# Kernel tuning notes

Measured on AMD Instinct MI355X. Metric: run time of the kernel, lower is better.

The kernel has to match this reference:

```python
import jax, jax.numpy as jnp
import numpy as np

N_VARS = 32        # n_variables
TEMPERATURE = 1.0  # softmax temperature (default)


def setup_inputs() -> dict:
    key = jax.random.key(0)
    k1, k2 = jax.random.split(key)
    B, C, T = 16, 3072, 2048  # C = n_var * (hidden_dim + n_var) = 32*(64+32)
    x = jax.random.normal(k1, (B, C, T), dtype=jnp.float32)
    x_instant = jax.random.normal(k2, (B, C, T), dtype=jnp.float32)
    return {"x": x, "x_instant": x_instant}


def _split_context_attention(v, n):
    B, _, T = v.shape
    v = v.reshape(B, n, -1, T)          # (B, n, hidden+n, T)
    attn = v[:, :, :n, :]               # (B, n, n, T) attention logits
    ctx = v[:, :, n:, :]                # (B, n, hidden, T)
    return ctx, attn


def reference(x, x_instant):
    n = N_VARS
    B, _, T = x.shape
    ctx, attn = _split_context_attention(x, n)
    ctx_i, attn_i = _split_context_attention(x_instant, n)
    ctx = jnp.concatenate([ctx, ctx_i], axis=-3)     # (B, 2n, hidden, T)
    attn = jnp.concatenate([attn, attn_i], axis=-2)  # (B, n, 2n, T)
    attn = jax.nn.softmax(attn / TEMPERATURE, axis=-2)
    # aggregate contexts with attention weights
    out = jnp.einsum('bijt,bjdt->bidt', attn, ctx)   # (B, n, hidden, T)
    out = out.reshape(B, -1, T)                      # (B, n*hidden, T)
    # ConvertInstant: zero the instantaneous self-edge (j = n + i), then sum chunks
    a1 = attn[:, :, :n, :]
    a2 = attn[:, :, n:, :]
    diag = jnp.eye(n, dtype=bool)[None, :, :, None]  # (1, n, n, 1)
    a2 = jnp.where(diag, jnp.zeros((), dtype=attn.dtype), a2)
    attentions = a1 + a2                             # (B, n, n, T)
    return out, attentions
```

## Files before the change

kernel.cpp:

```cpp
#include <hip/hip_runtime.h>
#include <stdint.h>


typedef unsigned int uint_t;
typedef float  f32x4   __attribute__((ext_vector_type(4)));
typedef short  short8v __attribute__((ext_vector_type(8)));

#define SYNCX() asm volatile("s_waitcnt lgkmcnt(0)\n\ts_barrier" ::: "memory")

constexpr int Bq = 16, Cq = 3072, Tq = 2048;
constexpr int TT = 32, TILES = 64, NBLK = Bq * TILES;
constexpr size_t ATT_OFF = (size_t)Bq * 2048 * Tq;
constexpr int TBS = 4224;
constexpr int LDS_BYTES = 135168;

__global__ __launch_bounds__(1024, 1) void attn_v14(const float* __restrict__ x,
                                                    const float* __restrict__ xi,
                                                    float* __restrict__ out)
{
    __shared__ __align__(16) unsigned char smem[LDS_BYTES];
    uint_t*    LW = (uint_t*)smem;
    uint64_t*  LQ = (uint64_t*)smem;
    float*     LF = (float*)smem;

    const int tid  = (int)threadIdx.x;
    const int b    = (int)blockIdx.x >> 6;
    const int tile = (int)blockIdx.x & (TILES - 1);
    const int t0   = tile * TT;
    const int tl   = tid & 31;
    const int slot = tid >> 5;

    const float* xb  = x  + (size_t)b * Cq * Tq + t0 + tl;
    const float* xib = xi + (size_t)b * Cq * Tq + t0 + tl;

    uint_t pk[32];
    float  cre[32];

    auto issue = [&](int c) {
        const int dh = c >> 1, jh = c & 1;
        const float* src = (jh == 0) ? x : xi;
        const float* sp  = src + (size_t)b * Cq * Tq
                         + (size_t)(32 + dh * 32 + slot) * Tq + t0 + tl;
#pragma unroll
        for (int kk = 0; kk < 32; ++kk) cre[kk] = sp[(size_t)kk * 96 * Tq];
    };

    {
        const int i = slot;
        float p[64];
#pragma unroll
        for (int j = 0; j < 32; ++j) p[j]      = xb [(size_t)(i * 96 + j) * Tq];
#pragma unroll
        for (int j = 0; j < 32; ++j) p[j + 32] = xib[(size_t)(i * 96 + j) * Tq];

        issue(0);

        float m = p[0];
#pragma unroll
        for (int j = 1; j < 64; ++j) m = fmaxf(m, p[j]);
        float s = 0.f;
#pragma unroll
        for (int j = 0; j < 64; ++j) { p[j] = __expf(p[j] - m); s += p[j]; }
        const float inv = 1.f / s;
#pragma unroll
        for (int j = 0; j < 64; ++j) p[j] *= inv;

        float* ao = out + ATT_OFF + ((size_t)(b * 32 + i) * 32) * Tq + t0 + tl;
#pragma unroll
        for (int j = 0; j < 32; ++j) {
            float v = p[j] + ((j == i) ? 0.f : p[j + 32]);
            __builtin_nontemporal_store(v, &ao[(size_t)j * Tq]);
        }
#pragma unroll
        for (int k = 0; k < 32; ++k) {
            uint_t b0 = __float_as_uint(p[2 * k]);
            uint_t b1 = __float_as_uint(p[2 * k + 1]);
            uint_t lo = (b0 + 0x7fffu + ((b0 >> 16) & 1u)) >> 16;
            uint_t hi = (b1 + 0x7fffu + ((b1 >> 16) & 1u)) >> 16;
            pk[k] = lo | (hi << 16);
        }
    }

    const int fw  = ((slot >> 2) & 3) ^ (slot & 3);
    const int TBw = tl * TBS + (tl & 7) * 16;

    const int l   = tid & 63;
    const int wv  = tid >> 6;
    const int frd = ((l >> 2) & 3) ^ (l & 3);
    const int kbr = (((l >> 4) ^ frd) & 3) * 16;
    const int rA  = (l & 15) * 64;

    auto stageP = [&](int jh) {
#pragma unroll
        for (int m = 0; m < 16; m += 2) {
            const int kbx  = (m >> 2) ^ fw;
            const int byte = TBw + slot * 64 + kbx * 16 + ((2 * m) & 7) * 2;
            uint64_t w = (uint64_t)pk[jh * 16 + m] |
                         ((uint64_t)pk[jh * 16 + m + 1] << 32);
            LQ[byte >> 3] = w;
        }
    };
    auto stageC = [&]() {
#pragma unroll
        for (int kk = 0; kk < 32; kk += 2) {
            uint_t b0 = __float_as_uint(cre[kk]);
            uint_t b1 = __float_as_uint(cre[kk + 1]);
            uint_t h0 = (b0 + 0x7fffu + ((b0 >> 16) & 1u)) >> 16;
            uint_t h1 = (b1 + 0x7fffu + ((b1 >> 16) & 1u)) >> 16;
            const int kbx  = (kk >> 3) ^ fw;
            const int byte = TBw + 2048 + slot * 64 + kbx * 16 + (kk & 7) * 2;
            LW[byte >> 2] = h0 | (h1 << 16);
        }
    };

    f32x4 acc[2][2][2];
    auto accClr = [&]() {
#pragma unroll
        for (int q = 0; q < 2; ++q)
#pragma unroll
            for (int s = 0; s < 2; ++s)
#pragma unroll
                for (int dt = 0; dt < 2; ++dt) acc[q][s][dt] = (f32x4)(0.f);
    };
    auto mfmaChunk = [&]() {
#pragma unroll
        for (int q = 0; q < 2; ++q) {
            const int tloc = 2 * wv + q;
            const int base = tloc * TBS + (tloc & 7) * 16;
            const short8v A0 = *(const short8v*)(smem + base        + rA + kbr);
            const short8v A1 = *(const short8v*)(smem + base + 1024 + rA + kbr);
            const short8v B0 = *(const short8v*)(smem + base + 2048 + rA + kbr);
            const short8v B1 = *(const short8v*)(smem + base + 3072 + rA + kbr);
            acc[q][0][0] = __builtin_amdgcn_mfma_f32_16x16x32_bf16(A0, B0, acc[q][0][0], 0, 0, 0);
            acc[q][0][1] = __builtin_amdgcn_mfma_f32_16x16x32_bf16(A0, B1, acc[q][0][1], 0, 0, 0);
            acc[q][1][0] = __builtin_amdgcn_mfma_f32_16x16x32_bf16(A1, B0, acc[q][1][0], 0, 0, 0);
            acc[q][1][1] = __builtin_amdgcn_mfma_f32_16x16x32_bf16(A1, B1, acc[q][1][1], 0, 0, 0);
        }
    };
    auto dump = [&](int dh) {
#pragma unroll
        for (int q = 0; q < 2; ++q)
#pragma unroll
            for (int s = 0; s < 2; ++s)
#pragma unroll
                for (int dt = 0; dt < 2; ++dt)
#pragma unroll
                    for (int ri = 0; ri < 4; ++ri) {
                        const int ii = s * 16 + (l >> 4) * 4 + ri;
                        const int dl = dt * 16 + (l & 15);
                        LF[(ii * 32 + dl) * 33 + 2 * wv + q] = acc[q][s][dt][ri];
                    }
        SYNCX();
        float* ob = out + (size_t)b * 2048 * Tq + t0 + tl;
#pragma unroll 8
        for (int kk = 0; kk < 32; ++kk) {
            const int ch = kk * 64 + dh * 32 + slot;
            __builtin_nontemporal_store(LF[(kk * 32 + slot) * 33 + tl],
                                        &ob[(size_t)ch * Tq]);
        }
        SYNCX();
    };

    accClr();
    stageP(0); stageC();
    SYNCX();
    issue(1);
    mfmaChunk();
    SYNCX();
    stageP(1); stageC();
    SYNCX();
    issue(2);
    mfmaChunk();
    SYNCX();
    dump(0);
    accClr();
    stageP(0); stageC();
    SYNCX();
    issue(3);
    mfmaChunk();
    SYNCX();
    stageP(1); stageC();
    SYNCX();
    mfmaChunk();
    SYNCX();
    dump(1);
}

extern "C" void kernel_launch(void* const* d_in, const int* in_sizes, int n_in,
                              void* d_out, int out_size, void* d_ws, size_t ws_size,
                              hipStream_t stream) {
    const float* x  = (const float*)d_in[0];
    const float* xi = (const float*)d_in[1];
    float* out = (float*)d_out;
    attn_v14<<<dim3(NBLK), dim3(1024), 0, stream>>>(x, xi, out);
}
```

Baseline: 258.9 us.

## Double-buffer LDS staging by time-half to overlap staging with MFMA

Splits the 32 time columns into two halves of 16 and stages each half into a separate LDS buffer, so one half can be written while MFMAs read the other half. Each wave now handles one time column per half instead of two consecutive ones, and the accumulator index maps to the time half. The aim is to hide LDS staging latency and the barrier stalls between staging and compute. In exchange there are more barriers and the staging work per step is split across half the threads, which leaves the other threads idle during those stores.

Measured after the change: 275.9 us. 1.07x slower.

```diff
diff --git a/kernel.cpp b/kernel.cpp
--- a/kernel.cpp
+++ b/kernel.cpp
@@ -12,9 +12,10 @@
 constexpr int TT = 32, TILES = 64, NBLK = Bq * TILES;
 constexpr size_t ATT_OFF = (size_t)Bq * 2048 * Tq;
 constexpr int TBS = 4224;
-constexpr int LDS_BYTES = 135168;
-
-__global__ __launch_bounds__(1024, 1) void attn_v14(const float* __restrict__ x,
+constexpr int BB  = 16 * TBS;
+constexpr int LDS_BYTES = 2 * BB;
+
+__global__ __launch_bounds__(1024, 1) void attn_v16(const float* __restrict__ x,
                                                     const float* __restrict__ xi,
                                                     float* __restrict__ out)
 {
@@ -36,8 +37,8 @@
     uint_t pk[32];
     float  cre[32];
 
-    auto issue = [&](int c) {
-        const int dh = c >> 1, jh = c & 1;
+    auto issueQ = [&](int q) {
+        const int dh = q >> 1, jh = q & 1;
         const float* src = (jh == 0) ? x : xi;
         const float* sp  = src + (size_t)b * Cq * Tq
                          + (size_t)(32 + dh * 32 + slot) * Tq + t0 + tl;
@@ -53,7 +54,7 @@
 #pragma unroll
         for (int j = 0; j < 32; ++j) p[j + 32] = xib[(size_t)(i * 96 + j) * Tq];
 
-        issue(0);
+        issueQ(0);
 
         float m = p[0];
 #pragma unroll
@@ -82,25 +83,30 @@
     }
 
     const int fw  = ((slot >> 2) & 3) ^ (slot & 3);
-    const int TBw = tl * TBS + (tl & 7) * 16;
+    const int tau = tl & 15;
+    const int thh = tl >> 4;
+    const int TBw = tau * TBS + (tau & 7) * 16;
 
     const int l   = tid & 63;
     const int wv  = tid >> 6;
     const int frd = ((l >> 2) & 3) ^ (l & 3);
     const int kbr = (((l >> 4) ^ frd) & 3) * 16;
     const int rA  = (l & 15) * 64;
-
-    auto stageP = [&](int jh) {
+    const int mb  = wv * TBS + (wv & 7) * 16;
+
+    auto stageP = [&](int jh, int th, int buf) {
+        if (thh != th) return;
 #pragma unroll
         for (int m = 0; m < 16; m += 2) {
             const int kbx  = (m >> 2) ^ fw;
-            const int byte = TBw + slot * 64 + kbx * 16 + ((2 * m) & 7) * 2;
+            const int byte = buf * BB + TBw + slot * 64 + kbx * 16 + ((2 * m) & 7) * 2;
             uint64_t w = (uint64_t)pk[jh * 16 + m] |
                          ((uint64_t)pk[jh * 16 + m + 1] << 32);
             LQ[byte >> 3] = w;
         }
     };
-    auto stageC = [&]() {
+    auto stageC = [&](int th, int buf) {
+        if (thh != th) return;
 #pragma unroll
         for (int kk = 0; kk < 32; kk += 2) {
             uint_t b0 = __float_as_uint(cre[kk]);
@@ -108,7 +114,7 @@
             uint_t h0 = (b0 + 0x7fffu + ((b0 >> 16) & 1u)) >> 16;
             uint_t h1 = (b1 + 0x7fffu + ((b1 >> 16) & 1u)) >> 16;
             const int kbx  = (kk >> 3) ^ fw;
-            const int byte = TBw + 2048 + slot * 64 + kbx * 16 + (kk & 7) * 2;
+            const int byte = buf * BB + TBw + 2048 + slot * 64 + kbx * 16 + (kk & 7) * 2;
             LW[byte >> 2] = h0 | (h1 << 16);
         }
     };
@@ -122,24 +128,20 @@
 #pragma unroll
                 for (int dt = 0; dt < 2; ++dt) acc[q][s][dt] = (f32x4)(0.f);
     };
-    auto mfmaChunk = [&]() {
-#pragma unroll
-        for (int q = 0; q < 2; ++q) {
-            const int tloc = 2 * wv + q;
-            const int base = tloc * TBS + (tloc & 7) * 16;
-            const short8v A0 = *(const short8v*)(smem + base        + rA + kbr);
-            const short8v A1 = *(const short8v*)(smem + base + 1024 + rA + kbr);
-            const short8v B0 = *(const short8v*)(smem + base + 2048 + rA + kbr);
-            const short8v B1 = *(const short8v*)(smem + base + 3072 + rA + kbr);
-            acc[q][0][0] = __builtin_amdgcn_mfma_f32_16x16x32_bf16(A0, B0, acc[q][0][0], 0, 0, 0);
-            acc[q][0][1] = __builtin_amdgcn_mfma_f32_16x16x32_bf16(A0, B1, acc[q][0][1], 0, 0, 0);
-            acc[q][1][0] = __builtin_amdgcn_mfma_f32_16x16x32_bf16(A1, B0, acc[q][1][0], 0, 0, 0);
-            acc[q][1][1] = __builtin_amdgcn_mfma_f32_16x16x32_bf16(A1, B1, acc[q][1][1], 0, 0, 0);
-        }
-    };
-    auto dump = [&](int dh) {
-#pragma unroll
-        for (int q = 0; q < 2; ++q)
+    auto mfmaC = [&](int th, int buf) {
+        const int base = buf * BB + mb;
+        const short8v A0 = *(const short8v*)(smem + base        + rA + kbr);
+        const short8v A1 = *(const short8v*)(smem + base + 1024 + rA + kbr);
+        const short8v B0 = *(const short8v*)(smem + base + 2048 + rA + kbr);
+        const short8v B1 = *(const short8v*)(smem + base + 3072 + rA + kbr);
+        acc[th][0][0] = __builtin_amdgcn_mfma_f32_16x16x32_bf16(A0, B0, acc[th][0][0], 0, 0, 0);
+        acc[th][0][1] = __builtin_amdgcn_mfma_f32_16x16x32_bf16(A0, B1, acc[th][0][1], 0, 0, 0);
+        acc[th][1][0] = __builtin_amdgcn_mfma_f32_16x16x32_bf16(A1, B0, acc[th][1][0], 0, 0, 0);
+        acc[th][1][1] = __builtin_amdgcn_mfma_f32_16x16x32_bf16(A1, B1, acc[th][1][1], 0, 0, 0);
+    };
+    auto dumpW = [&]() {
+#pragma unroll
+        for (int th = 0; th < 2; ++th)
 #pragma unroll
             for (int s = 0; s < 2; ++s)
 #pragma unroll
@@ -148,9 +150,10 @@
                     for (int ri = 0; ri < 4; ++ri) {
                         const int ii = s * 16 + (l >> 4) * 4 + ri;
                         const int dl = dt * 16 + (l & 15);
-                        LF[(ii * 32 + dl) * 33 + 2 * wv + q] = acc[q][s][dt][ri];
+                        LF[(ii * 32 + dl) * 33 + th * 16 + wv] = acc[th][s][dt][ri];
                     }
-        SYNCX();
+    };
+    auto dumpS = [&](int dh) {
         float* ob = out + (size_t)b * 2048 * Tq + t0 + tl;
 #pragma unroll 8
         for (int kk = 0; kk < 32; ++kk) {
@@ -158,32 +161,41 @@
             __builtin_nontemporal_store(LF[(kk * 32 + slot) * 33 + tl],
                                         &ob[(size_t)ch * Tq]);
         }
-        SYNCX();
     };
 
     accClr();
-    stageP(0); stageC();
-    SYNCX();
-    issue(1);
-    mfmaChunk();
-    SYNCX();
-    stageP(1); stageC();
-    SYNCX();
-    issue(2);
-    mfmaChunk();
-    SYNCX();
-    dump(0);
+    stageP(0, 0, 0); stageC(0, 0);
+    SYNCX();
+    stageP(0, 1, 1); stageC(1, 1);
+    issueQ(1);
+    mfmaC(0, 0);
+    SYNCX();
+    stageP(1, 0, 0); stageC(0, 0);
+    mfmaC(1, 1);
+    SYNCX();
+    stageP(1, 1, 1); stageC(1, 1);
+    issueQ(2);
+    mfmaC(0, 0);
+    SYNCX();
+    mfmaC(1, 1);
+    SYNCX();
+    dumpW(); SYNCX(); dumpS(0); SYNCX();
     accClr();
-    stageP(0); stageC();
-    SYNCX();
-    issue(3);
-    mfmaChunk();
-    SYNCX();
-    stageP(1); stageC();
-    SYNCX();
-    mfmaChunk();
-    SYNCX();
-    dump(1);
+    stageP(0, 0, 0); stageC(0, 0);
+    SYNCX();
+    stageP(0, 1, 1); stageC(1, 1);
+    issueQ(3);
+    mfmaC(0, 0);
+    SYNCX();
+    stageP(1, 0, 0); stageC(0, 0);
+    mfmaC(1, 1);
+    SYNCX();
+    stageP(1, 1, 1); stageC(1, 1);
+    mfmaC(0, 0);
+    SYNCX();
+    mfmaC(1, 1);
+    SYNCX();
+    dumpW(); SYNCX(); dumpS(1);
 }
 
 extern "C" void kernel_launch(void* const* d_in, const int* in_sizes, int n_in,
@@ -192,5 +204,5 @@
     const float* x  = (const float*)d_in[0];
     const float* xi = (const float*)d_in[1];
     float* out = (float*)d_out;
-    attn_v14<<<dim3(NBLK), dim3(1024), 0, stream>>>(x, xi, out);
+    attn_v16<<<dim3(NBLK), dim3(1024), 0, stream>>>(x, xi, out);
 }
```

## Make kernel persistent with 512 threads processing four tiles and prefetching logits

Applied to the files above, without the earlier changes.

Shrinks the grid to 256 blocks of 512 threads. Each block loops over four (batch, time-tile) units, and each thread handles two attention rows and two context channels per stage. The next tile's logits are prefetched during the last MFMA stage to overlap global loads with compute, and fewer blocks cut launch and tail costs. In exchange, register pressure per thread roughly doubles, there are fewer waves per CU to hide latency, and the first stageC loads cre from x for both halves before issueQ reloads it.

After: 400.1 us. +54.5%, slower.

```diff
diff --git a/kernel.cpp b/kernel.cpp
--- a/kernel.cpp
+++ b/kernel.cpp
@@ -9,14 +9,15 @@
 #define SYNCX() asm volatile("s_waitcnt lgkmcnt(0)\n\ts_barrier" ::: "memory")
 
 constexpr int Bq = 16, Cq = 3072, Tq = 2048;
-constexpr int TT = 32, TILES = 64, NBLK = Bq * TILES;
+constexpr int TT = 32, TILES = 64;
+constexpr int NBLK = 256;
 constexpr size_t ATT_OFF = (size_t)Bq * 2048 * Tq;
 constexpr int TBS = 4224;
 constexpr int LDS_BYTES = 135168;
 
-__global__ __launch_bounds__(1024, 1) void attn_v14(const float* __restrict__ x,
-                                                    const float* __restrict__ xi,
-                                                    float* __restrict__ out)
+__global__ __launch_bounds__(512, 1) void attn_v17(const float* __restrict__ x,
+                                                   const float* __restrict__ xi,
+                                                   float* __restrict__ out)
 {
     __shared__ __align__(16) unsigned char smem[LDS_BYTES];
     uint_t*    LW = (uint_t*)smem;
@@ -24,62 +25,9 @@
     float*     LF = (float*)smem;
 
     const int tid  = (int)threadIdx.x;
-    const int b    = (int)blockIdx.x >> 6;
-    const int tile = (int)blockIdx.x & (TILES - 1);
-    const int t0   = tile * TT;
     const int tl   = tid & 31;
     const int slot = tid >> 5;
-
-    const float* xb  = x  + (size_t)b * Cq * Tq + t0 + tl;
-    const float* xib = xi + (size_t)b * Cq * Tq + t0 + tl;
-
-    uint_t pk[32];
-    float  cre[32];
-
-    auto issue = [&](int c) {
-        const int dh = c >> 1, jh = c & 1;
-        const float* src = (jh == 0) ? x : xi;
-        const float* sp  = src + (size_t)b * Cq * Tq
-                         + (size_t)(32 + dh * 32 + slot) * Tq + t0 + tl;
-#pragma unroll
-        for (int kk = 0; kk < 32; ++kk) cre[kk] = sp[(size_t)kk * 96 * Tq];
-    };
-
-    {
-        const int i = slot;
-        float p[64];
-#pragma unroll
-        for (int j = 0; j < 32; ++j) p[j]      = xb [(size_t)(i * 96 + j) * Tq];
-#pragma unroll
-        for (int j = 0; j < 32; ++j) p[j + 32] = xib[(size_t)(i * 96 + j) * Tq];
-
-        issue(0);
-
-        float m = p[0];
-#pragma unroll
-        for (int j = 1; j < 64; ++j) m = fmaxf(m, p[j]);
-        float s = 0.f;
-#pragma unroll
-        for (int j = 0; j < 64; ++j) { p[j] = __expf(p[j] - m); s += p[j]; }
-        const float inv = 1.f / s;
-#pragma unroll
-        for (int j = 0; j < 64; ++j) p[j] *= inv;
-
-        float* ao = out + ATT_OFF + ((size_t)(b * 32 + i) * 32) * Tq + t0 + tl;
-#pragma unroll
-        for (int j = 0; j < 32; ++j) {
-            float v = p[j] + ((j == i) ? 0.f : p[j + 32]);
-            __builtin_nontemporal_store(v, &ao[(size_t)j * Tq]);
-        }
-#pragma unroll
-        for (int k = 0; k < 32; ++k) {
-            uint_t b0 = __float_as_uint(p[2 * k]);
-            uint_t b1 = __float_as_uint(p[2 * k + 1]);
-            uint_t lo = (b0 + 0x7fffu + ((b0 >> 16) & 1u)) >> 16;
-            uint_t hi = (b1 + 0x7fffu + ((b1 >> 16) & 1u)) >> 16;
-            pk[k] = lo | (hi << 16);
-        }
-    }
+    const int blk  = (int)blockIdx.x;
 
     const int fw  = ((slot >> 2) & 3) ^ (slot & 3);
     const int TBw = tl * TBS + (tl & 7) * 16;
@@ -90,100 +38,222 @@
     const int kbr = (((l >> 4) ^ frd) & 3) * 16;
     const int rA  = (l & 15) * 64;
 
-    auto stageP = [&](int jh) {
-#pragma unroll
-        for (int m = 0; m < 16; m += 2) {
-            const int kbx  = (m >> 2) ^ fw;
-            const int byte = TBw + slot * 64 + kbx * 16 + ((2 * m) & 7) * 2;
-            uint64_t w = (uint64_t)pk[jh * 16 + m] |
-                         ((uint64_t)pk[jh * 16 + m + 1] << 32);
-            LQ[byte >> 3] = w;
-        }
-    };
-    auto stageC = [&]() {
-#pragma unroll
-        for (int kk = 0; kk < 32; kk += 2) {
-            uint_t b0 = __float_as_uint(cre[kk]);
-            uint_t b1 = __float_as_uint(cre[kk + 1]);
-            uint_t h0 = (b0 + 0x7fffu + ((b0 >> 16) & 1u)) >> 16;
-            uint_t h1 = (b1 + 0x7fffu + ((b1 >> 16) & 1u)) >> 16;
-            const int kbx  = (kk >> 3) ^ fw;
-            const int byte = TBw + 2048 + slot * 64 + kbx * 16 + (kk & 7) * 2;
-            LW[byte >> 2] = h0 | (h1 << 16);
-        }
-    };
-
-    f32x4 acc[2][2][2];
-    auto accClr = [&]() {
-#pragma unroll
-        for (int q = 0; q < 2; ++q)
-#pragma unroll
-            for (int s = 0; s < 2; ++s)
-#pragma unroll
-                for (int dt = 0; dt < 2; ++dt) acc[q][s][dt] = (f32x4)(0.f);
-    };
-    auto mfmaChunk = [&]() {
-#pragma unroll
-        for (int q = 0; q < 2; ++q) {
-            const int tloc = 2 * wv + q;
-            const int base = tloc * TBS + (tloc & 7) * 16;
-            const short8v A0 = *(const short8v*)(smem + base        + rA + kbr);
-            const short8v A1 = *(const short8v*)(smem + base + 1024 + rA + kbr);
-            const short8v B0 = *(const short8v*)(smem + base + 2048 + rA + kbr);
-            const short8v B1 = *(const short8v*)(smem + base + 3072 + rA + kbr);
-            acc[q][0][0] = __builtin_amdgcn_mfma_f32_16x16x32_bf16(A0, B0, acc[q][0][0], 0, 0, 0);
-            acc[q][0][1] = __builtin_amdgcn_mfma_f32_16x16x32_bf16(A0, B1, acc[q][0][1], 0, 0, 0);
-            acc[q][1][0] = __builtin_amdgcn_mfma_f32_16x16x32_bf16(A1, B0, acc[q][1][0], 0, 0, 0);
-            acc[q][1][1] = __builtin_amdgcn_mfma_f32_16x16x32_bf16(A1, B1, acc[q][1][1], 0, 0, 0);
-        }
-    };
-    auto dump = [&](int dh) {
-#pragma unroll
-        for (int q = 0; q < 2; ++q)
-#pragma unroll
-            for (int s = 0; s < 2; ++s)
-#pragma unroll
-                for (int dt = 0; dt < 2; ++dt)
-#pragma unroll
-                    for (int ri = 0; ri < 4; ++ri) {
-                        const int ii = s * 16 + (l >> 4) * 4 + ri;
-                        const int dl = dt * 16 + (l & 15);
-                        LF[(ii * 32 + dl) * 33 + 2 * wv + q] = acc[q][s][dt][ri];
-                    }
-        SYNCX();
-        float* ob = out + (size_t)b * 2048 * Tq + t0 + tl;
+    float  p0[64], p1[64];
+    uint_t pk0[32], pk1[32];
+    float  cre[64];
+    f32x4  acc[4][2][2];
+
+    {
+        const int n = blk * 4;
+        const int b0 = n >> 6, t00 = (n & 63) * TT;
+        const float* xb  = x  + (size_t)b0 * Cq * Tq + t00 + tl;
+        const float* xib = xi + (size_t)b0 * Cq * Tq + t00 + tl;
+#pragma unroll
+        for (int j = 0; j < 32; ++j) p0[j]      = xb [(size_t)(slot * 96 + j) * Tq];
+#pragma unroll
+        for (int j = 0; j < 32; ++j) p0[j + 32] = xib[(size_t)(slot * 96 + j) * Tq];
+    }
+
+#pragma unroll 1
+    for (int s = 0; s < 4; ++s) {
+        const int n  = blk * 4 + s;
+        const int b  = n >> 6;
+        const int t0 = (n & 63) * TT;
+        const float* xb  = x  + (size_t)b * Cq * Tq + t0 + tl;
+        const float* xib = xi + (size_t)b * Cq * Tq + t0 + tl;
+
+        {
+            const int i = slot;
+            float m = p0[0];
+#pragma unroll
+            for (int j = 1; j < 64; ++j) m = fmaxf(m, p0[j]);
+            float sm = 0.f;
+#pragma unroll
+            for (int j = 0; j < 64; ++j) { p0[j] = __expf(p0[j] - m); sm += p0[j]; }
+            const float inv = 1.f / sm;
+#pragma unroll
+            for (int j = 0; j < 64; ++j) p0[j] *= inv;
+
+#pragma unroll
+            for (int j = 0; j < 32; ++j) p1[j]      = xb [(size_t)((slot + 16) * 96 + j) * Tq];
+#pragma unroll
+            for (int j = 0; j < 32; ++j) p1[j + 32] = xib[(size_t)((slot + 16) * 96 + j) * Tq];
+
+            float* ao = out + ATT_OFF + ((size_t)(b * 32 + i) * 32) * Tq + t0 + tl;
+#pragma unroll
+            for (int j = 0; j < 32; ++j) {
+                float v = p0[j] + ((j == i) ? 0.f : p0[j + 32]);
+                __builtin_nontemporal_store(v, &ao[(size_t)j * Tq]);
+            }
+#pragma unroll
+            for (int k = 0; k < 32; ++k) {
+                uint_t b0_ = __float_as_uint(p0[2 * k]);
+                uint_t b1_ = __float_as_uint(p0[2 * k + 1]);
+                uint_t lo = (b0_ + 0x7fffu + ((b0_ >> 16) & 1u)) >> 16;
+                uint_t hi = (b1_ + 0x7fffu + ((b1_ >> 16) & 1u)) >> 16;
+                pk0[k] = lo | (hi << 16);
+            }
+        }
+
+        {
+            const float* sp0 = x + (size_t)b * Cq * Tq + (size_t)(32 + slot) * Tq + t0 + tl;
+            const float* sp1 = x + (size_t)b * Cq * Tq + (size_t)(32 + slot + 16) * Tq + t0 + tl;
+#pragma unroll
+            for (int kk = 0; kk < 32; ++kk) cre[kk]      = sp0[(size_t)kk * 96 * Tq];
+#pragma unroll
+            for (int kk = 0; kk < 32; ++kk) cre[kk + 32] = sp1[(size_t)kk * 96 * Tq];
+        }
+
+        {
+            const int i = slot + 16;
+            float m = p1[0];
+#pragma unroll
+            for (int j = 1; j < 64; ++j) m = fmaxf(m, p1[j]);
+            float sm = 0.f;
+#pragma unroll
+            for (int j = 0; j < 64; ++j) { p1[j] = __expf(p1[j] - m); sm += p1[j]; }
+            const float inv = 1.f / sm;
+#pragma unroll
+            for (int j = 0; j < 64; ++j) p1[j] *= inv;
+
+            float* ao = out + ATT_OFF + ((size_t)(b * 32 + i) * 32) * Tq + t0 + tl;
+#pragma unroll
+            for (int j = 0; j < 32; ++j) {
+                float v = p1[j] + ((j == i) ? 0.f : p1[j + 32]);
+                __builtin_nontemporal_store(v, &ao[(size_t)j * Tq]);
+            }
+#pragma unroll
+            for (int k = 0; k < 32; ++k) {
+                uint_t b0_ = __float_as_uint(p1[2 * k]);
+                uint_t b1_ = __float_as_uint(p1[2 * k + 1]);
+                uint_t lo = (b0_ + 0x7fffu + ((b0_ >> 16) & 1u)) >> 16;
+                uint_t hi = (b1_ + 0x7fffu + ((b1_ >> 16) & 1u)) >> 16;
+                pk1[k] = lo | (hi << 16);
+            }
+        }
+
+        auto issueQ = [&](int q) {
+            const int dh = q >> 1, jh = q & 1;
+            const float* src = (jh == 0) ? x : xi;
+            const float* sp0 = src + (size_t)b * Cq * Tq
+                             + (size_t)(32 + dh * 32 + slot) * Tq + t0 + tl;
+            const float* sp1 = sp0 + (size_t)16 * Tq;
+#pragma unroll
+            for (int kk = 0; kk < 32; ++kk) cre[kk]      = sp0[(size_t)kk * 96 * Tq];
+#pragma unroll
+            for (int kk = 0; kk < 32; ++kk) cre[kk + 32] = sp1[(size_t)kk * 96 * Tq];
+        };
+        auto stageP = [&](int jh) {
+#pragma unroll
+            for (int m = 0; m < 16; m += 2) {
+                const int kbx  = (m >> 2) ^ fw;
+                const int byte = TBw + slot * 64 + kbx * 16 + ((2 * m) & 7) * 2;
+                LQ[byte >> 3] = (uint64_t)pk0[jh * 16 + m] |
+                                ((uint64_t)pk0[jh * 16 + m + 1] << 32);
+                const int byte2 = byte + 16 * 64;
+                LQ[byte2 >> 3] = (uint64_t)pk1[jh * 16 + m] |
+                                 ((uint64_t)pk1[jh * 16 + m + 1] << 32);
+            }
+        };
+        auto stageC = [&]() {
+#pragma unroll
+            for (int kk = 0; kk < 32; kk += 2) {
+                const int kbx  = (kk >> 3) ^ fw;
+                uint_t a0 = __float_as_uint(cre[kk]);
+                uint_t a1 = __float_as_uint(cre[kk + 1]);
+                uint_t h0 = (a0 + 0x7fffu + ((a0 >> 16) & 1u)) >> 16;
+                uint_t h1 = (a1 + 0x7fffu + ((a1 >> 16) & 1u)) >> 16;
+                const int byte = TBw + 2048 + slot * 64 + kbx * 16 + (kk & 7) * 2;
+                LW[byte >> 2] = h0 | (h1 << 16);
+                uint_t c0 = __float_as_uint(cre[kk + 32]);
+                uint_t c1 = __float_as_uint(cre[kk + 33]);
+                uint_t g0 = (c0 + 0x7fffu + ((c0 >> 16) & 1u)) >> 16;
+                uint_t g1 = (c1 + 0x7fffu + ((c1 >> 16) & 1u)) >> 16;
+                const int byte2 = byte + 16 * 64;
+                LW[byte2 >> 2] = g0 | (g1 << 16);
+            }
+        };
+        auto accClr = [&]() {
+#pragma unroll
+            for (int q = 0; q < 4; ++q)
+#pragma unroll
+                for (int s_ = 0; s_ < 2; ++s_)
+#pragma unroll
+                    for (int dt = 0; dt < 2; ++dt) acc[q][s_][dt] = (f32x4)(0.f);
+        };
+        auto mfmaChunk = [&]() {
+#pragma unroll
+            for (int q = 0; q < 4; ++q) {
+                const int tloc = 4 * wv + q;
+                const int base = tloc * TBS + (tloc & 7) * 16;
+                const short8v A0 = *(const short8v*)(smem + base        + rA + kbr);
+                const short8v A1 = *(const short8v*)(smem + base + 1024 + rA + kbr);
+                const short8v B0 = *(const short8v*)(smem + base + 2048 + rA + kbr);
+                const short8v B1 = *(const short8v*)(smem + base + 3072 + rA + kbr);
+                acc[q][0][0] = __builtin_amdgcn_mfma_f32_16x16x32_bf16(A0, B0, acc[q][0][0], 0, 0, 0);
+                acc[q][0][1] = __builtin_amdgcn_mfma_f32_16x16x32_bf16(A0, B1, acc[q][0][1], 0, 0, 0);
+                acc[q][1][0] = __builtin_amdgcn_mfma_f32_16x16x32_bf16(A1, B0, acc[q][1][0], 0, 0, 0);
+                acc[q][1][1] = __builtin_amdgcn_mfma_f32_16x16x32_bf16(A1, B1, acc[q][1][1], 0, 0, 0);
+            }
+        };
+        auto dump = [&](int dh) {
+#pragma unroll
+            for (int q = 0; q < 4; ++q)
+#pragma unroll
+                for (int s_ = 0; s_ < 2; ++s_)
+#pragma unroll
+                    for (int dt = 0; dt < 2; ++dt)
+#pragma unroll
+                        for (int ri = 0; ri < 4; ++ri) {
+                            const int ii = s_ * 16 + (l >> 4) * 4 + ri;
+                            const int dl = dt * 16 + (l & 15);
+                            LF[(ii * 32 + dl) * 33 + 4 * wv + q] = acc[q][s_][dt][ri];
+                        }
+            SYNCX();
+            float* ob = out + (size_t)b * 2048 * Tq + t0 + tl;
 #pragma unroll 8
-        for (int kk = 0; kk < 32; ++kk) {
-            const int ch = kk * 64 + dh * 32 + slot;
-            __builtin_nontemporal_store(LF[(kk * 32 + slot) * 33 + tl],
-                                        &ob[(size_t)ch * Tq]);
-        }
-        SYNCX();
-    };
-
-    accClr();
-    stageP(0); stageC();
-    SYNCX();
-    issue(1);
-    mfmaChunk();
-    SYNCX();
-    stageP(1); stageC();
-    SYNCX();
-    issue(2);
-    mfmaChunk();
-    SYNCX();
-    dump(0);
-    accClr();
-    stageP(0); stageC();
-    SYNCX();
-    issue(3);
-    mfmaChunk();
-    SYNCX();
-    stageP(1); stageC();
-    SYNCX();
-    mfmaChunk();
-    SYNCX();
-    dump(1);
+            for (int kk = 0; kk < 32; ++kk) {
+                const int ch  = kk * 64 + dh * 32 + slot;
+                __builtin_nontemporal_store(LF[(kk * 32 + slot) * 33 + tl],
+                                            &ob[(size_t)ch * Tq]);
+                const int ch2 = ch + 16;
+                __builtin_nontemporal_store(LF[(kk * 32 + slot + 16) * 33 + tl],
+                                            &ob[(size_t)ch2 * Tq]);
+            }
+            SYNCX();
+        };
+
+        accClr();
+        stageP(0); stageC();
+        SYNCX();
+        issueQ(1); mfmaChunk();
+        SYNCX();
+        stageP(1); stageC();
+        SYNCX();
+        issueQ(2); mfmaChunk();
+        SYNCX();
+        dump(0);
+        accClr();
+        stageP(0); stageC();
+        SYNCX();
+        issueQ(3); mfmaChunk();
+        SYNCX();
+        stageP(1); stageC();
+        if (s < 3) {
+            const int n1 = blk * 4 + s + 1;
+            const int b1 = n1 >> 6, t01 = (n1 & 63) * TT;
+            const float* xb1  = x  + (size_t)b1 * Cq * Tq + t01 + tl;
+            const float* xib1 = xi + (size_t)b1 * Cq * Tq + t01 + tl;
+#pragma unroll
+            for (int j = 0; j < 32; ++j) p0[j]      = xb1 [(size_t)(slot * 96 + j) * Tq];
+#pragma unroll
+            for (int j = 0; j < 32; ++j) p0[j + 32] = xib1[(size_t)(slot * 96 + j) * Tq];
+        }
+        SYNCX();
+        mfmaChunk();
+        SYNCX();
+        dump(1);
+    }
 }
 
 extern "C" void kernel_launch(void* const* d_in, const int* in_sizes, int n_in,
@@ -192,5 +262,5 @@
     const float* x  = (const float*)d_in[0];
     const float* xi = (const float*)d_in[1];
     float* out = (float*)d_out;
-    attn_v14<<<dim3(NBLK), dim3(1024), 0, stream>>>(x, xi, out);
+    attn_v17<<<dim3(NBLK), dim3(512), 0, stream>>>(x, xi, out);
 }
```
